# Optimization experiments

Measured on AMD Instinct MI355X. Metric: run time of the kernel, lower is better.

The kernel has to match this reference:

```python
import jax, jax.numpy as jnp
import numpy as np

NUM_FEATURES = 35
BLANK = 2          # local blank index inside each 3-way category
NEG = -1e30        # finite stand-in for -inf (keeps grads NaN-free)


def _ctc_losses(log_probs, ext, skip_ok, valid, input_lengths, target_lengths):
    """Batched CTC negative log-likelihood.
    log_probs: [T,B,F,3] log-softmax per category
    ext:       [B,F,L] extended label sequence (blank interleaved), L=2S+1
    skip_ok:   [B,F,L] whether the l-2 transition is allowed
    valid:     [B,F,L] positions within 2*target_len+1
    Returns per-(B,F) loss.
    """
    T = log_probs.shape[0]

    emit0 = jnp.take_along_axis(log_probs[0], ext, axis=-1)  # [B,F,L]
    alpha = jnp.full_like(emit0, NEG)
    alpha = alpha.at[..., 0].set(emit0[..., 0])
    alpha = alpha.at[..., 1].set(jnp.where(target_lengths > 0, emit0[..., 1], NEG))

    pad1 = jnp.full(alpha.shape[:-1] + (1,), NEG, alpha.dtype)
    pad2 = jnp.full(alpha.shape[:-1] + (2,), NEG, alpha.dtype)

    def step(alpha, xs):
        lp_t, t = xs                                   # lp_t: [B,F,3]
        emit = jnp.take_along_axis(lp_t, ext, axis=-1)  # [B,F,L]
        a1 = jnp.concatenate([pad1, alpha[..., :-1]], axis=-1)
        a2 = jnp.concatenate([pad2, alpha[..., :-2]], axis=-1)
        prev = jnp.logaddexp(jnp.logaddexp(alpha, a1),
                             jnp.where(skip_ok, a2, NEG))
        new = jnp.where(valid, prev + emit, NEG)
        active = (t < input_lengths)[:, None, None]     # [B,1,1]
        return jnp.where(active, new, alpha), None

    alpha, _ = jax.lax.scan(step, alpha, (log_probs[1:], jnp.arange(1, T)))

    idx_last = 2 * target_lengths                       # [B,F] final blank
    last = jnp.take_along_axis(alpha, idx_last[..., None], axis=-1)[..., 0]
    prev_ = jnp.take_along_axis(alpha, jnp.maximum(idx_last - 1, 0)[..., None], axis=-1)[..., 0]
    prev_ = jnp.where(target_lengths > 0, prev_, NEG)
    ll = jnp.logaddexp(last, prev_)
    # zero_infinity=True: impossible alignments contribute 0 loss
    return jnp.where(ll > -1e29, -ll, 0.0)


def reference(logits, targets, input_lengths, target_lengths):
    # logits: [T,B,71]; targets: [B,35,S] local labels in {0,1};
    # input_lengths: [B]; target_lengths: [B,35]
    T, B, _ = logits.shape
    F = NUM_FEATURES
    pos = logits[:, :, :F]
    neg = logits[:, :, F:2 * F]
    blank = jnp.broadcast_to(logits[:, :, 2 * F:2 * F + 1], pos.shape)
    lp = jax.nn.log_softmax(jnp.stack([pos, neg, blank], axis=-1), axis=-1)  # [T,B,F,3]

    S = targets.shape[-1]
    L = 2 * S + 1
    ext = jnp.full((B, F, L), BLANK, jnp.int32).at[:, :, 1::2].set(targets.astype(jnp.int32))
    posL = jnp.arange(L)
    valid = posL[None, None, :] < (2 * target_lengths[..., None] + 1)
    ext_m2 = jnp.pad(ext[:, :, :-2], ((0, 0), (0, 0), (2, 0)), constant_values=BLANK)
    skip_ok = (ext != BLANK) & (ext != ext_m2) & (posL[None, None, :] >= 2)

    loss_bf = _ctc_losses(lp, ext, skip_ok, valid, input_lengths, target_lengths)  # [B,F]
    # reduction='mean': per-sample loss divided by its target length, averaged over batch,
    # then summed over the 35 feature categories (the python loop accumulates per-feature means)
    tl = jnp.maximum(target_lengths, 1).astype(loss_bf.dtype)
    return jnp.sum(jnp.mean(loss_bf / tl, axis=0))


def setup_inputs() -> dict:
    T, B, S = 600, 32, 80
    key = jax.random.key(0)
    k1, k2, k3 = jax.random.split(key, 3)
    logits = jax.random.normal(k1, (T, B, 2 * NUM_FEATURES + 1), dtype=jnp.float32)
    targets = jax.random.randint(k2, (B, NUM_FEATURES, S), 0, 2, dtype=jnp.int32)
    target_lengths = jax.random.randint(k3, (B, NUM_FEATURES), 40, S + 1, dtype=jnp.int32)
    input_lengths = jnp.full((B,), T, dtype=jnp.int32)
    return {"logits": logits, "targets": targets,
            "input_lengths": input_lengths, "target_lengths": target_lengths}
```

## Files before the change

kernel.cpp:

```cpp
#include <hip/hip_runtime.h>

#define LN2 0.6931471805599453f

__device__ __forceinline__ float dpp_shr1_zero(float x) {
    return __int_as_float(__builtin_amdgcn_update_dpp(
        0, __float_as_int(x), 0x138, 0xF, 0xF, true));
}
__device__ __forceinline__ int dpp_shr1_keep(int x) {
    return __builtin_amdgcn_update_dpp(x, x, 0x138, 0xF, 0xF, false);
}
__device__ __forceinline__ float exp2i_clamped(int d) {
    int k = 127 + d;
    k = (k < 1) ? 1 : ((k > 254) ? 254 : k);
    return __uint_as_float(((unsigned)k) << 23);
}
__device__ __forceinline__ float sel3(int e, float v0, float v1, float v2) {
    return (e == 2) ? v2 : ((e == 1) ? v1 : v0);
}

struct CtcState {
    float a0, a1, a2;
    float s1;
    float k0, k1;
    int   esum;
};

__device__ __forceinline__ void ctc_step(float em0, float em1, float em2,
                                         CtcState& st, float skm2) {
    float d2 = dpp_shr1_zero(st.a2);
    float d1 = dpp_shr1_zero(st.a1);
    float n0 = fmaf(st.k0, d1, fmaf(st.s1, d2, st.a0)) * em0;
    float n1 = fmaf(st.k1, d2, st.a1 + st.a0) * em1;
    float n2 = fmaf(skm2, st.a0, st.a2 + st.a1) * em2;
    st.a0 = n0; st.a1 = n1; st.a2 = n2;
}

__device__ __forceinline__ void ctc_rescale(CtcState& st, float skm0, float skm1) {
    float m = fmaxf(fmaxf(st.a0, st.a1), st.a2);
    int ebits = (int)(__float_as_uint(m) >> 23);
    bool dead = (ebits == 0);
    int de = dead ? 0 : (127 - ebits);
    float scz = dead ? 0.0f : exp2i_clamped(de);
    st.a0 *= scz; st.a1 *= scz; st.a2 *= scz;
    st.esum -= de;
    #pragma unroll
    for (int r = 0; r < 5; ++r) {
        int en = dpp_shr1_keep(st.esum);
        st.esum = dead ? en : st.esum;
    }
    int enf = dpp_shr1_keep(st.esum);
    int gap = enf - st.esum;
    int adj = (gap > 64) ? (gap - 64) : 0;
    float sc3 = exp2i_clamped(-adj);
    st.a0 *= sc3; st.a1 *= sc3; st.a2 *= sc3;
    st.esum += adj;
    st.s1 = exp2i_clamped(gap - adj);
    st.k0 = skm0 * st.s1;
    st.k1 = skm1 * st.s1;
}

__global__ __launch_bounds__(64, 1) void ctc_kernel(
    const float* __restrict__ logits,
    const int* __restrict__ targets,
    const int* __restrict__ input_lengths,
    const int* __restrict__ target_lengths,
    float* __restrict__ loss_out,
    int T, int B, int Ff, int S)
{
    const int p = blockIdx.x;
    const int b = p / Ff;
    const int f = p - b * Ff;
    const int lane = (int)threadIdx.x;
    const int C = 2 * Ff + 1;
    const int L = 2 * S + 1;

    const int tl = target_lengths[p];
    const int il = input_lengths[b];
    const int tbase = p * S;

    int e0i, e1i, e2i;
    float skm0, skm1, skm2;
    {
        int e[3]; float sk[3];
        const int l0 = 3 * lane;
        #pragma unroll
        for (int j = 0; j < 3; ++j) {
            int l = l0 + j;
            int ev = 2; float sok = 0.f;
            if (l < L && (l & 1)) {
                int s = (l - 1) >> 1;
                ev = targets[tbase + s];
                if (s >= 1) sok = (targets[tbase + s - 1] != ev) ? 1.f : 0.f;
            }
            e[j] = ev; sk[j] = sok;
        }
        e0i = e[0]; e1i = e[1]; e2i = e[2];
        skm0 = sk[0]; skm1 = sk[1]; skm2 = sk[2];
    }

    __shared__ float4 slp[608];
    {
        const float* lg = logits + (size_t)b * C;
        const size_t strideT = (size_t)B * C;
        float c0 = 0.f, c1 = 0.f, c2 = 0.f;
        if (lane < T) {
            const float* r = lg + (size_t)lane * strideT;
            c0 = r[f]; c1 = r[Ff + f]; c2 = r[2 * Ff];
        }
        #pragma unroll 1
        for (int j = 0; j < 10; ++j) {
            int i = lane + (j << 6);
            int inx = i + 64;
            float n0 = 0.f, n1 = 0.f, n2 = 0.f;
            if (inx < T) {
                const float* r = lg + (size_t)inx * strideT;
                n0 = r[f]; n1 = r[Ff + f]; n2 = r[2 * Ff];
            }
            float4 v = make_float4(0.f, 0.f, 0.f, 0.f);
            if (i < T) {
                float m = fmaxf(fmaxf(c0, c1), c2);
                float ep = __expf(c0 - m);
                float en = __expf(c1 - m);
                float eb = __expf(c2 - m);
                float inv = __builtin_amdgcn_rcpf(ep + en + eb);
                v = make_float4(ep * inv, en * inv, eb * inv, 0.f);
            }
            if (i < 608) slp[i] = v;
            c0 = n0; c1 = n1; c2 = n2;
        }
    }
    __syncthreads();

    const char* base8 = (const char*)slp;
    const char* qt0 = base8 + (e0i << 2);
    const char* qt1 = base8 + (e1i << 2);
    const char* qt2 = base8 + (e2i << 2);

    CtcState st;
    {
        float4 E0 = slp[0];
        st.a0 = (lane == 0) ? E0.z : 0.f;
        st.a1 = (lane == 0 && tl > 0) ? sel3(e1i, E0.x, E0.y, E0.z) : 0.f;
        st.a2 = 0.f;
        st.s1 = 1.f; st.k0 = skm0; st.k1 = skm1;
        st.esum = 0;
    }

    const int t_end = (il < T) ? il : T;

    const char* pr0 = qt0 + 16;
    const char* pr1 = qt1 + 16;
    const char* pr2 = qt2 + 16;
#define LDE(OFF, E) { E[0] = *(const float*)(pr0 + (OFF)); \
                      E[1] = *(const float*)(pr1 + (OFF)); \
                      E[2] = *(const float*)(pr2 + (OFF)); }
    float A0[3], A1[3], A2[3], A3[3], B0[3], B1[3], B2[3], B3[3];
    float C0[3], C1[3], C2[3], C3[3], D0[3], D1[3], D2[3], D3[3];
    LDE(  0, A0); LDE( 16, A1); LDE( 32, A2); LDE( 48, A3);
    LDE( 64, B0); LDE( 80, B1); LDE( 96, B2); LDE(112, B3);
    LDE(128, C0); LDE(144, C1); LDE(160, C2); LDE(176, C3);
    LDE(192, D0); LDE(208, D1); LDE(224, D2); LDE(240, D3);
    int t = 1;
    for (; t + 15 < t_end; t += 16) {
        ctc_rescale(st, skm0, skm1);
        ctc_step(A0[0], A0[1], A0[2], st, skm2);
        ctc_step(A1[0], A1[1], A1[2], st, skm2);
        ctc_step(A2[0], A2[1], A2[2], st, skm2);
        ctc_step(A3[0], A3[1], A3[2], st, skm2);
        LDE(256, A0); LDE(272, A1); LDE(288, A2); LDE(304, A3);
        ctc_step(B0[0], B0[1], B0[2], st, skm2);
        ctc_step(B1[0], B1[1], B1[2], st, skm2);
        ctc_step(B2[0], B2[1], B2[2], st, skm2);
        ctc_step(B3[0], B3[1], B3[2], st, skm2);
        LDE(320, B0); LDE(336, B1); LDE(352, B2); LDE(368, B3);
        ctc_rescale(st, skm0, skm1);
        ctc_step(C0[0], C0[1], C0[2], st, skm2);
        ctc_step(C1[0], C1[1], C1[2], st, skm2);
        ctc_step(C2[0], C2[1], C2[2], st, skm2);
        ctc_step(C3[0], C3[1], C3[2], st, skm2);
        LDE(384, C0); LDE(400, C1); LDE(416, C2); LDE(432, C3);
        ctc_step(D0[0], D0[1], D0[2], st, skm2);
        ctc_step(D1[0], D1[1], D1[2], st, skm2);
        ctc_step(D2[0], D2[1], D2[2], st, skm2);
        ctc_step(D3[0], D3[1], D3[2], st, skm2);
        LDE(448, D0); LDE(464, D1); LDE(480, D2); LDE(496, D3);
        pr0 += 256; pr1 += 256; pr2 += 256;
    }
#undef LDE
    for (; t < t_end; ++t) {
        int o = t << 4;
        float e0 = *(const float*)(qt0 + o);
        float e1 = *(const float*)(qt1 + o);
        float e2 = *(const float*)(qt2 + o);
        ctc_step(e0, e1, e2, st, skm2);
    }

    __shared__ float sa[192];
    __shared__ int   se[64];
    {
        int l = 3 * lane;
        sa[l] = st.a0; sa[l + 1] = st.a1; sa[l + 2] = st.a2;
        se[lane] = st.esum;
    }
    __syncthreads();
    if (lane == 0) {
        int l1 = 2 * tl;
        int l2 = (tl > 0) ? (2 * tl - 1) : 0;
        float v1 = sa[l1];
        float v2 = (tl > 0) ? sa[l2] : 0.f;
        int e1 = se[l1 / 3];
        int e2 = (tl > 0) ? se[l2 / 3] : 0;
        int em_ = (e1 > e2) ? e1 : e2;
        float sum = ldexpf(v1, e1 - em_) + ldexpf(v2, e2 - em_);
        float ll = (__log2f(sum) + (float)em_) * LN2;
        float loss = (ll > -1e29f) ? -ll : 0.0f;
        float denom = (tl > 0) ? (float)tl : 1.0f;
        loss_out[p] = loss / denom;
    }
}

__global__ __launch_bounds__(256) void reduce_kernel(
    const float* __restrict__ v, float* __restrict__ out, int n, float invB)
{
    __shared__ float buf[256];
    float s = 0.f;
    for (int i = (int)threadIdx.x; i < n; i += 256) s += v[i];
    buf[threadIdx.x] = s;
    __syncthreads();
    for (int off = 128; off > 0; off >>= 1) {
        if ((int)threadIdx.x < off) buf[threadIdx.x] += buf[threadIdx.x + off];
        __syncthreads();
    }
    if (threadIdx.x == 0) out[0] = buf[0] * invB;
}

extern "C" void kernel_launch(void* const* d_in, const int* in_sizes, int n_in,
                              void* d_out, int out_size, void* d_ws, size_t ws_size,
                              hipStream_t stream) {
    const float* logits         = (const float*)d_in[0];
    const int*   targets        = (const int*)d_in[1];
    const int*   input_lengths  = (const int*)d_in[2];
    const int*   target_lengths = (const int*)d_in[3];
    float* out = (float*)d_out;

    const int B  = in_sizes[2];
    const int BF = in_sizes[3];
    const int Ff = BF / B;
    const int S  = in_sizes[1] / BF;
    const int C  = 2 * Ff + 1;
    const int T  = in_sizes[0] / (B * C);

    float* losses = (float*)d_ws;

    ctc_kernel<<<BF, 64, 0, stream>>>(logits, targets, input_lengths,
                                      target_lengths, losses, T, B, Ff, S);
    reduce_kernel<<<1, 256, 0, stream>>>(losses, out, BF, 1.0f / (float)B);
}
```

Before: 54.61 us.

## Split CTC recursion into concurrent forward and backward passes meeting midway

Runs a forward alpha pass and a backward beta pass at the same time, each covering about half the time steps, with their steps interleaved. The likelihood is then recovered from a dot product of alpha and beta at the midpoint. This halves the length of the serial dependency chain and gives the scheduler two independent chains to overlap. In exchange it doubles the per-step arithmetic and register use and adds more complex rescaling and combination logic, which carries some numerical risk.

```diff
diff --git a/kernel.cpp b/kernel.cpp
--- a/kernel.cpp
+++ b/kernel.cpp
@@ -8,6 +8,13 @@
 }
 __device__ __forceinline__ int dpp_shr1_keep(int x) {
     return __builtin_amdgcn_update_dpp(x, x, 0x138, 0xF, 0xF, false);
+}
+__device__ __forceinline__ float dpp_shl1_zero(float x) {
+    return __int_as_float(__builtin_amdgcn_update_dpp(
+        0, __float_as_int(x), 0x130, 0xF, 0xF, true));
+}
+__device__ __forceinline__ int dpp_shl1_keep(int x) {
+    return __builtin_amdgcn_update_dpp(x, x, 0x130, 0xF, 0xF, false);
 }
 __device__ __forceinline__ float exp2i_clamped(int d) {
     int k = 127 + d;
@@ -18,15 +25,19 @@
     return (e == 2) ? v2 : ((e == 1) ? v1 : v0);
 }
 
-struct CtcState {
+struct FwdState {
     float a0, a1, a2;
-    float s1;
-    float k0, k1;
+    float s1, k0, k1;
     int   esum;
 };
-
-__device__ __forceinline__ void ctc_step(float em0, float em1, float em2,
-                                         CtcState& st, float skm2) {
+struct BwdState {
+    float c0, c1, c2;
+    float s1b, kA, kB;
+    int   esum;
+};
+
+__device__ __forceinline__ void fwd_step(float em0, float em1, float em2,
+                                         FwdState& st, float skm2) {
     float d2 = dpp_shr1_zero(st.a2);
     float d1 = dpp_shr1_zero(st.a1);
     float n0 = fmaf(st.k0, d1, fmaf(st.s1, d2, st.a0)) * em0;
@@ -34,8 +45,17 @@
     float n2 = fmaf(skm2, st.a0, st.a2 + st.a1) * em2;
     st.a0 = n0; st.a1 = n1; st.a2 = n2;
 }
-
-__device__ __forceinline__ void ctc_rescale(CtcState& st, float skm0, float skm1) {
+__device__ __forceinline__ void bwd_step(float em0, float em1, float em2,
+                                         BwdState& st, float skm2) {
+    float d3 = dpp_shl1_zero(st.c0);
+    float d4 = dpp_shl1_zero(st.c1);
+    float n0 = fmaf(skm2, st.c2, st.c0 + st.c1) * em0;
+    float n1 = fmaf(st.kA, d3, st.c1 + st.c2) * em1;
+    float n2 = fmaf(st.kB, d4, fmaf(st.s1b, d3, st.c2)) * em2;
+    st.c0 = n0; st.c1 = n1; st.c2 = n2;
+}
+
+__device__ __forceinline__ void fwd_rescale(FwdState& st, float skm0, float skm1) {
     float m = fmaxf(fmaxf(st.a0, st.a1), st.a2);
     int ebits = (int)(__float_as_uint(m) >> 23);
     bool dead = (ebits == 0);
@@ -57,6 +77,39 @@
     st.s1 = exp2i_clamped(gap - adj);
     st.k0 = skm0 * st.s1;
     st.k1 = skm1 * st.s1;
+}
+__device__ __forceinline__ void bwd_rescale(BwdState& st, float sknA, float sknB) {
+    float m = fmaxf(fmaxf(st.c0, st.c1), st.c2);
+    int ebits = (int)(__float_as_uint(m) >> 23);
+    bool dead = (ebits == 0);
+    int de = dead ? 0 : (127 - ebits);
+    float scz = dead ? 0.0f : exp2i_clamped(de);
+    st.c0 *= scz; st.c1 *= scz; st.c2 *= scz;
+    st.esum -= de;
+    #pragma unroll
+    for (int r = 0; r < 5; ++r) {
+        int en = dpp_shl1_keep(st.esum);
+        st.esum = dead ? en : st.esum;
+    }
+    #pragma unroll
+    for (int r = 0; r < 3; ++r) {
+        int enl = dpp_shr1_keep(st.esum);
+        int mn = (enl < st.esum) ? enl : st.esum;
+        st.esum = dead ? mn : st.esum;
+    }
+    int deadR = dpp_shl1_keep(dead ? 1 : 0);
+    int enf = dpp_shl1_keep(st.esum);
+    int gap = enf - st.esum;
+    int adj = (gap > 64) ? (gap - 64) : 0;
+    adj = (adj > 126) ? 126 : adj;
+    adj = deadR ? 0 : adj;
+    float sc3 = exp2i_clamped(-adj);
+    st.c0 *= sc3; st.c1 *= sc3; st.c2 *= sc3;
+    st.esum += adj;
+    float s1b = exp2i_clamped(gap - adj);
+    st.s1b = deadR ? 0.f : s1b;
+    st.kA = sknA * st.s1b;
+    st.kB = sknB * st.s1b;
 }
 
 __global__ __launch_bounds__(64, 1) void ctc_kernel(
@@ -97,6 +150,8 @@
         e0i = e[0]; e1i = e[1]; e2i = e[2];
         skm0 = sk[0]; skm1 = sk[1]; skm2 = sk[2];
     }
+    const float sknA = dpp_shl1_zero(skm0);
+    const float sknB = dpp_shl1_zero(skm1);
 
     __shared__ float4 slp[608];
     {
@@ -136,84 +191,158 @@
     const char* qt1 = base8 + (e1i << 2);
     const char* qt2 = base8 + (e2i << 2);
 
-    CtcState st;
+    const int TL = (il < T) ? il : T;
+    const int m_ = (TL >= 2) ? ((TL - 1) >> 1) : 0;
+    const int Bk = (TL >= 2) ? (TL - 2 - m_) : 0;
+    const int F  = m_;
+    const int P  = (F < Bk) ? F : Bk;
+    const int nblk = P >> 3;
+
+    FwdState fs;
+    BwdState bs;
     {
         float4 E0 = slp[0];
-        st.a0 = (lane == 0) ? E0.z : 0.f;
-        st.a1 = (lane == 0 && tl > 0) ? sel3(e1i, E0.x, E0.y, E0.z) : 0.f;
-        st.a2 = 0.f;
-        st.s1 = 1.f; st.k0 = skm0; st.k1 = skm1;
-        st.esum = 0;
-    }
-
-    const int t_end = (il < T) ? il : T;
-
-    const char* pr0 = qt0 + 16;
-    const char* pr1 = qt1 + 16;
-    const char* pr2 = qt2 + 16;
-#define LDE(OFF, E) { E[0] = *(const float*)(pr0 + (OFF)); \
-                      E[1] = *(const float*)(pr1 + (OFF)); \
-                      E[2] = *(const float*)(pr2 + (OFF)); }
-    float A0[3], A1[3], A2[3], A3[3], B0[3], B1[3], B2[3], B3[3];
-    float C0[3], C1[3], C2[3], C3[3], D0[3], D1[3], D2[3], D3[3];
-    LDE(  0, A0); LDE( 16, A1); LDE( 32, A2); LDE( 48, A3);
-    LDE( 64, B0); LDE( 80, B1); LDE( 96, B2); LDE(112, B3);
-    LDE(128, C0); LDE(144, C1); LDE(160, C2); LDE(176, C3);
-    LDE(192, D0); LDE(208, D1); LDE(224, D2); LDE(240, D3);
-    int t = 1;
-    for (; t + 15 < t_end; t += 16) {
-        ctc_rescale(st, skm0, skm1);
-        ctc_step(A0[0], A0[1], A0[2], st, skm2);
-        ctc_step(A1[0], A1[1], A1[2], st, skm2);
-        ctc_step(A2[0], A2[1], A2[2], st, skm2);
-        ctc_step(A3[0], A3[1], A3[2], st, skm2);
-        LDE(256, A0); LDE(272, A1); LDE(288, A2); LDE(304, A3);
-        ctc_step(B0[0], B0[1], B0[2], st, skm2);
-        ctc_step(B1[0], B1[1], B1[2], st, skm2);
-        ctc_step(B2[0], B2[1], B2[2], st, skm2);
-        ctc_step(B3[0], B3[1], B3[2], st, skm2);
-        LDE(320, B0); LDE(336, B1); LDE(352, B2); LDE(368, B3);
-        ctc_rescale(st, skm0, skm1);
-        ctc_step(C0[0], C0[1], C0[2], st, skm2);
-        ctc_step(C1[0], C1[1], C1[2], st, skm2);
-        ctc_step(C2[0], C2[1], C2[2], st, skm2);
-        ctc_step(C3[0], C3[1], C3[2], st, skm2);
-        LDE(384, C0); LDE(400, C1); LDE(416, C2); LDE(432, C3);
-        ctc_step(D0[0], D0[1], D0[2], st, skm2);
-        ctc_step(D1[0], D1[1], D1[2], st, skm2);
-        ctc_step(D2[0], D2[1], D2[2], st, skm2);
-        ctc_step(D3[0], D3[1], D3[2], st, skm2);
-        LDE(448, D0); LDE(464, D1); LDE(480, D2); LDE(496, D3);
-        pr0 += 256; pr1 += 256; pr2 += 256;
-    }
-#undef LDE
-    for (; t < t_end; ++t) {
-        int o = t << 4;
-        float e0 = *(const float*)(qt0 + o);
-        float e1 = *(const float*)(qt1 + o);
-        float e2 = *(const float*)(qt2 + o);
-        ctc_step(e0, e1, e2, st, skm2);
+        fs.a0 = (lane == 0) ? E0.z : 0.f;
+        fs.a1 = (lane == 0 && tl > 0) ? sel3(e1i, E0.x, E0.y, E0.z) : 0.f;
+        fs.a2 = 0.f;
+        fs.s1 = 1.f; fs.k0 = skm0; fs.k1 = skm1;
+        fs.esum = 0;
+
+        int oTL = (TL - 1) << 4;
+        float eL0 = *(const float*)(qt0 + oTL);
+        float eL1 = *(const float*)(qt1 + oTL);
+        float eL2 = *(const float*)(qt2 + oTL);
+        int l0i = 3 * lane;
+        int end1 = 2 * tl, end2 = 2 * tl - 1;
+        bs.c0 = (l0i == end1 || l0i == end2) ? eL0 : 0.f;
+        bs.c1 = (l0i + 1 == end1 || l0i + 1 == end2) ? eL1 : 0.f;
+        bs.c2 = (l0i + 2 == end1 || l0i + 2 == end2) ? eL2 : 0.f;
+        bs.s1b = 1.f; bs.kA = sknA; bs.kB = sknB;
+        bs.esum = 0;
+    }
+
+    const char* pf0 = qt0 + 16;
+    const char* pf1 = qt1 + 16;
+    const char* pf2 = qt2 + 16;
+    const char* pb0 = qt0 + ((TL - 2) << 4);
+    const char* pb1 = qt1 + ((TL - 2) << 4);
+    const char* pb2 = qt2 + ((TL - 2) << 4);
+#define LDF(OFF, E) { E[0] = *(const float*)(pf0 + (OFF)); \
+                      E[1] = *(const float*)(pf1 + (OFF)); \
+                      E[2] = *(const float*)(pf2 + (OFF)); }
+#define LDB(OFF, E) { E[0] = *(const float*)(pb0 - (OFF)); \
+                      E[1] = *(const float*)(pb1 - (OFF)); \
+                      E[2] = *(const float*)(pb2 - (OFF)); }
+    float FA0[3], FA1[3], FA2[3], FA3[3], FB0[3], FB1[3], FB2[3], FB3[3];
+    float GA0[3], GA1[3], GA2[3], GA3[3], GB0[3], GB1[3], GB2[3], GB3[3];
+    if (nblk > 0) {
+        LDF(  0, FA0); LDF( 16, FA1); LDF( 32, FA2); LDF( 48, FA3);
+        LDF( 64, FB0); LDF( 80, FB1); LDF( 96, FB2); LDF(112, FB3);
+        LDB(  0, GA0); LDB( 16, GA1); LDB( 32, GA2); LDB( 48, GA3);
+        LDB( 64, GB0); LDB( 80, GB1); LDB( 96, GB2); LDB(112, GB3);
+    }
+    for (int blk = 0; blk < nblk; ++blk) {
+        fwd_rescale(fs, skm0, skm1);
+        bwd_rescale(bs, sknA, sknB);
+        fwd_step(FA0[0], FA0[1], FA0[2], fs, skm2);
+        bwd_step(GA0[0], GA0[1], GA0[2], bs, skm2);
+        fwd_step(FA1[0], FA1[1], FA1[2], fs, skm2);
+        bwd_step(GA1[0], GA1[1], GA1[2], bs, skm2);
+        fwd_step(FA2[0], FA2[1], FA2[2], fs, skm2);
+        bwd_step(GA2[0], GA2[1], GA2[2], bs, skm2);
+        fwd_step(FA3[0], FA3[1], FA3[2], fs, skm2);
+        bwd_step(GA3[0], GA3[1], GA3[2], bs, skm2);
+        LDF(128, FA0); LDF(144, FA1); LDF(160, FA2); LDF(176, FA3);
+        LDB(128, GA0); LDB(144, GA1); LDB(160, GA2); LDB(176, GA3);
+        fwd_step(FB0[0], FB0[1], FB0[2], fs, skm2);
+        bwd_step(GB0[0], GB0[1], GB0[2], bs, skm2);
+        fwd_step(FB1[0], FB1[1], FB1[2], fs, skm2);
+        bwd_step(GB1[0], GB1[1], GB1[2], bs, skm2);
+        fwd_step(FB2[0], FB2[1], FB2[2], fs, skm2);
+        bwd_step(GB2[0], GB2[1], GB2[2], bs, skm2);
+        fwd_step(FB3[0], FB3[1], FB3[2], fs, skm2);
+        bwd_step(GB3[0], GB3[1], GB3[2], bs, skm2);
+        LDF(192, FB0); LDF(208, FB1); LDF(224, FB2); LDF(240, FB3);
+        LDB(192, GB0); LDB(208, GB1); LDB(224, GB2); LDB(240, GB3);
+        pf0 += 128; pf1 += 128; pf2 += 128;
+        pb0 -= 128; pb1 -= 128; pb2 -= 128;
+    }
+#undef LDF
+#undef LDB
+    int tf = 8 * nblk + 1;
+    int tb = TL - 2 - 8 * nblk;
+    while (tf <= F && tb >= m_ + 1) {
+        int of = tf << 4, ob = tb << 4;
+        float f0 = *(const float*)(qt0 + of);
+        float f1 = *(const float*)(qt1 + of);
+        float f2 = *(const float*)(qt2 + of);
+        float g0 = *(const float*)(qt0 + ob);
+        float g1 = *(const float*)(qt1 + ob);
+        float g2 = *(const float*)(qt2 + ob);
+        fwd_step(f0, f1, f2, fs, skm2);
+        bwd_step(g0, g1, g2, bs, skm2);
+        ++tf; --tb;
+    }
+    while (tf <= F) {
+        int of = tf << 4;
+        float f0 = *(const float*)(qt0 + of);
+        float f1 = *(const float*)(qt1 + of);
+        float f2 = *(const float*)(qt2 + of);
+        fwd_step(f0, f1, f2, fs, skm2);
+        ++tf;
+    }
+    while (tb >= m_ + 1) {
+        int ob = tb << 4;
+        float g0 = *(const float*)(qt0 + ob);
+        float g1 = *(const float*)(qt1 + ob);
+        float g2 = *(const float*)(qt2 + ob);
+        bwd_step(g0, g1, g2, bs, skm2);
+        --tb;
     }
 
     __shared__ float sa[192];
-    __shared__ int   se[64];
-    {
-        int l = 3 * lane;
-        sa[l] = st.a0; sa[l + 1] = st.a1; sa[l + 2] = st.a2;
-        se[lane] = st.esum;
+    __shared__ float sg[194];
+    __shared__ int   seb[65];
+    __shared__ float sdot[64];
+    __shared__ int   sE[64];
+    {
+        int l0b = 3 * lane;
+        sa[l0b] = fs.a0; sa[l0b + 1] = fs.a1; sa[l0b + 2] = fs.a2;
+        sg[l0b] = bs.c0; sg[l0b + 1] = bs.c1; sg[l0b + 2] = bs.c2;
+        seb[lane] = bs.esum;
+        if (lane == 0) { sg[192] = 0.f; sg[193] = 0.f; seb[64] = 0; }
+    }
+    __syncthreads();
+    {
+        float scn = exp2i_clamped(seb[lane + 1] - bs.esum);
+        float g3 = sg[3 * lane + 3] * scn;
+        float g4 = sg[3 * lane + 4] * scn;
+        float s0 = fmaf(skm2, bs.c2, bs.c0 + bs.c1);
+        float s1 = fmaf(sknA, g3, bs.c1 + bs.c2);
+        float s2 = fmaf(sknB, g4, bs.c2 + g3);
+        float dot = fs.a0 * s0 + fs.a1 * s1 + fs.a2 * s2;
+        sdot[lane] = dot;
+        sE[lane] = fs.esum + bs.esum;
     }
     __syncthreads();
     if (lane == 0) {
-        int l1 = 2 * tl;
-        int l2 = (tl > 0) ? (2 * tl - 1) : 0;
-        float v1 = sa[l1];
-        float v2 = (tl > 0) ? sa[l2] : 0.f;
-        int e1 = se[l1 / 3];
-        int e2 = (tl > 0) ? se[l2 / 3] : 0;
-        int em_ = (e1 > e2) ? e1 : e2;
-        float sum = ldexpf(v1, e1 - em_) + ldexpf(v2, e2 - em_);
-        float ll = (__log2f(sum) + (float)em_) * LN2;
-        float loss = (ll > -1e29f) ? -ll : 0.0f;
+        float loss = 0.f;
+        if (TL == 1) {
+            float v = sa[2 * tl] + ((tl > 0) ? sa[2 * tl - 1] : 0.f);
+            if (v > 0.f) loss = -(__log2f(v) * LN2);
+        } else {
+            int Emax = -0x40000000;
+            for (int i = 0; i < 64; ++i)
+                if (sdot[i] > 0.f && sE[i] > Emax) Emax = sE[i];
+            if (Emax != -0x40000000) {
+                float sum = 0.f;
+                for (int i = 0; i < 64; ++i) {
+                    int d = sE[i] - Emax;
+                    if (d > -127 && sdot[i] > 0.f) sum += sdot[i] * exp2i_clamped(d);
+                }
+                loss = -((__log2f(sum) + (float)Emax) * LN2);
+            }
+        }
         float denom = (tl > 0) ? (float)tl : 1.0f;
         loss_out[p] = loss / denom;
     }
```

New measurement: 64.80 us. +18.7%, slower.
